# Kernel tuning notes

Hardware: AMD Instinct MI355X
Metric: run time of the kernel (lower is better)

## Reference

```python
import jax, jax.numpy as jnp
import numpy as np

B, S = 32, 4096
QRYDIM, CTXDIM, ENCDIM = 512, 512, 256


def setup_inputs() -> dict:
    key = jax.random.key(0)
    ks = jax.random.split(key, 8)
    qry = jax.random.normal(ks[0], (B, QRYDIM), dtype=jnp.float32)
    ctx = jax.random.normal(ks[1], (B, S, CTXDIM), dtype=jnp.float32)
    ctx_mask = jax.random.randint(ks[2], (B, S), 0, 2, dtype=jnp.int32)
    # first Linear(qrydim+ctxdim, encdim): split into ctx-part and qry-part
    # (equivalent to concat([ctx, qry]) @ W1^T since concat order is [ctx, qry])
    sc1 = 1.0 / np.sqrt(QRYDIM + CTXDIM)
    Wc = jax.random.uniform(ks[3], (CTXDIM, ENCDIM), jnp.float32, -sc1, sc1)
    Wq = jax.random.uniform(ks[4], (QRYDIM, ENCDIM), jnp.float32, -sc1, sc1)
    b1 = jax.random.uniform(ks[5], (ENCDIM,), jnp.float32, -sc1, sc1)
    sc2 = 1.0 / np.sqrt(ENCDIM)
    w2 = jax.random.uniform(ks[6], (ENCDIM,), jnp.float32, -sc2, sc2)
    b2 = jax.random.uniform(ks[7], (), jnp.float32, -sc2, sc2)
    return {"qry": qry, "ctx": ctx, "ctx_mask": ctx_mask,
            "Wc": Wc, "Wq": Wq, "b1": b1, "w2": w2, "b2": b2}


def reference(qry, ctx, ctx_mask, Wc, Wq, b1, w2, b2):
    # hidden = tanh(concat([ctx, qry_broadcast]) @ W1 + b1), computed without
    # materializing the (B, S, CTXDIM+QRYDIM) concat tensor
    h_ctx = jnp.einsum('bsc,ce->bse', ctx, Wc)          # (B, S, E)
    h_qry = jnp.einsum('bq,qe->be', qry, Wq)            # (B, E)
    h = jnp.tanh(h_ctx + h_qry[:, None, :] + b1)        # (B, S, E)
    scores = jnp.einsum('bse,e->bs', h, w2) + b2        # (B, S)
    # additive log-mask, then softmax over seqlen
    scores = scores + jnp.log(ctx_mask.astype(jnp.float32))
    alphas = jax.nn.softmax(scores, axis=-1)            # (B, S)
    # weighted sum over context (values default to ctx)
    summary = jnp.einsum('bs,bsd->bd', alphas, ctx)     # (B, CTXDIM)
    return alphas, summary, scores
```

## Files before the change

kernel.cpp:

```cpp
#include <hip/hip_runtime.h>
#include <math.h>

#define BB 32
#define SS 4096
#define CD 512
#define ED 256

#define ALPHAS_OFF 0
#define SUMMARY_OFF (BB * SS)
#define SCORES_OFF (BB * SS + BB * CD)

#define NEG_BIG (-1.0e30f)

typedef __attribute__((ext_vector_type(8))) short short8;
typedef __attribute__((ext_vector_type(8))) unsigned short us8;
typedef __attribute__((ext_vector_type(4))) float f32x4;

__device__ __forceinline__ unsigned short f2bf(float f) {
    unsigned u = __float_as_uint(f);
    u += 0x7FFFu + ((u >> 16) & 1u);
    return (unsigned short)(u >> 16);
}
__device__ __forceinline__ float bf2f(unsigned short h) {
    return __uint_as_float(((unsigned)h) << 16);
}
__device__ __forceinline__ float fast_tanh(float x) {
    const float ex = __expf(2.0f * x);
    return 1.0f - __fdividef(2.0f, ex + 1.0f);
}

#define WS_BH_OFF 32768
#define BPLANE 131072

__global__ void k_prep(const float* __restrict__ Wc, unsigned short* __restrict__ Bh,
                       unsigned short* __restrict__ Bl) {
    const int bid = blockIdx.x;
    const int l = threadIdx.x;
    const int e = (bid & 15) * 16 + (l & 15);
    const int kbase = (bid >> 4) * 32 + (l >> 4) * 8;
    const size_t off = ((size_t)bid * 64 + l) * 8;
#pragma unroll
    for (int j = 0; j < 8; ++j) {
        const float f = Wc[(size_t)(kbase + j) * ED + e];
        const unsigned short h = f2bf(f);
        Bh[off + j] = h;
        Bl[off + j] = f2bf(f - bf2f(h));
    }
}

__global__ void k_hq(const float* __restrict__ qry, const float* __restrict__ Wq,
                     const float* __restrict__ b1, float* __restrict__ hq) {
    const int b = blockIdx.x;
    const int e = threadIdx.x;
    __shared__ float qs[CD];
    qs[e] = qry[b * CD + e];
    qs[e + 256] = qry[b * CD + e + 256];
    __syncthreads();
    float acc = b1[e];
#pragma unroll 8
    for (int c = 0; c < CD; ++c) {
        acc = fmaf(qs[c], Wq[c * ED + e], acc);
    }
    hq[b * ED + e] = acc;
}

#define ST 64
__global__ __launch_bounds__(256, 3)
void k_scores(const float* __restrict__ ctx,
              const unsigned short* __restrict__ Bh, const unsigned short* __restrict__ Bl,
              const float* __restrict__ hq, const float* __restrict__ w2,
              const float* __restrict__ b2p, const int* __restrict__ mask,
              float* __restrict__ out) {
    const int b = blockIdx.y;
    const int s0 = blockIdx.x * ST;
    const int tid = threadIdx.x;
    const int w = tid >> 6;
    const int l = tid & 63;
    const int ehalf = w & 1;
    const int mhalf = w >> 1;

    __shared__ unsigned short AsH[2][4 * 64 * 8];
    __shared__ unsigned short AsL[2][4 * 64 * 8];
    __shared__ float red[2][ST];

    f32x4 acc[2][8];
#pragma unroll
    for (int mi = 0; mi < 2; ++mi)
#pragma unroll
        for (int t = 0; t < 8; ++t) acc[mi][t] = (f32x4)(0.0f);

    const float* ctx_b = ctx + (size_t)(b * SS + s0) * CD;

    const int amt = tid >> 6;
    const int alif = tid & 63;
    const int ar = amt * 16 + (alif & 15);
    const int akg = alif >> 4;
    const float* aptr = ctx_b + (size_t)ar * CD + akg * 8;

    const unsigned short* bhp = Bh + l * 8;
    const unsigned short* blp = Bl + l * 8;

    {
        const float4 v0 = *(const float4*)(aptr);
        const float4 v1 = *(const float4*)(aptr + 4);
        const float f[8] = {v0.x, v0.y, v0.z, v0.w, v1.x, v1.y, v1.z, v1.w};
        us8 H, L;
#pragma unroll
        for (int j = 0; j < 8; ++j) {
            const unsigned short h = f2bf(f[j]);
            H[j] = h;
            L[j] = f2bf(f[j] - bf2f(h));
        }
        *(us8*)(&AsH[0][tid * 8]) = H;
        *(us8*)(&AsL[0][tid * 8]) = L;
    }
    asm volatile("s_waitcnt lgkmcnt(0)" ::: "memory");
    __builtin_amdgcn_sched_barrier(0);
    __builtin_amdgcn_s_barrier();
    __builtin_amdgcn_sched_barrier(0);

    int cur = 0;
    for (int c = 0; c < 16; ++c) {
        float4 n0, n1;
        if (c < 15) {
            n0 = *(const float4*)(aptr + (c + 1) * 32);
            n1 = *(const float4*)(aptr + (c + 1) * 32 + 4);
        }

        short8 ah[2], alr[2];
#pragma unroll
        for (int mi = 0; mi < 2; ++mi) {
            const int aoff = ((mhalf * 2 + mi) * 64 + l) * 8;
            ah[mi] = *(const short8*)(&AsH[cur][aoff]);
            alr[mi] = *(const short8*)(&AsL[cur][aoff]);
        }

        __builtin_amdgcn_s_setprio(1);
#pragma unroll
        for (int et = 0; et < 8; ++et) {
            const int etile = ehalf * 8 + et;
            const size_t boff = (size_t)(c * 16 + etile) * 512;
            const short8 bh = *(const short8*)(bhp + boff);
            const short8 bl = *(const short8*)(blp + boff);
#pragma unroll
            for (int mi = 0; mi < 2; ++mi) {
                acc[mi][et] = __builtin_amdgcn_mfma_f32_16x16x32_bf16(ah[mi], bh, acc[mi][et], 0, 0, 0);
                acc[mi][et] = __builtin_amdgcn_mfma_f32_16x16x32_bf16(alr[mi], bh, acc[mi][et], 0, 0, 0);
                acc[mi][et] = __builtin_amdgcn_mfma_f32_16x16x32_bf16(ah[mi], bl, acc[mi][et], 0, 0, 0);
            }
        }
        __builtin_amdgcn_s_setprio(0);

        if (c < 15) {
            const float f[8] = {n0.x, n0.y, n0.z, n0.w, n1.x, n1.y, n1.z, n1.w};
            us8 H, L;
#pragma unroll
            for (int j = 0; j < 8; ++j) {
                const unsigned short h = f2bf(f[j]);
                H[j] = h;
                L[j] = f2bf(f[j] - bf2f(h));
            }
            *(us8*)(&AsH[cur ^ 1][tid * 8]) = H;
            *(us8*)(&AsL[cur ^ 1][tid * 8]) = L;
        }
        asm volatile("s_waitcnt lgkmcnt(0)" ::: "memory");
        __builtin_amdgcn_sched_barrier(0);
        __builtin_amdgcn_s_barrier();
        __builtin_amdgcn_sched_barrier(0);
        cur ^= 1;
    }

    float hqr[8], w2r[8];
#pragma unroll
    for (int t = 0; t < 8; ++t) {
        const int e = (ehalf * 8 + t) * 16 + (l & 15);
        hqr[t] = hq[b * ED + e];
        w2r[t] = w2[e];
    }

#pragma unroll
    for (int mi = 0; mi < 2; ++mi) {
#pragma unroll
        for (int reg = 0; reg < 4; ++reg) {
            float v = 0.0f;
#pragma unroll
            for (int t = 0; t < 8; ++t) {
                v += w2r[t] * fast_tanh(acc[mi][t][reg] + hqr[t]);
            }
            v += __shfl_xor(v, 1, 64);
            v += __shfl_xor(v, 2, 64);
            v += __shfl_xor(v, 4, 64);
            v += __shfl_xor(v, 8, 64);
            if ((l & 15) == 0) {
                const int row = (l >> 4) * 4 + reg;
                red[ehalf][(mhalf * 2 + mi) * 16 + row] = v;
            }
        }
    }
    __syncthreads();
    if (tid < ST) {
        const int s = s0 + tid;
        float sc = red[0][tid] + red[1][tid] + b2p[0];
        if (mask[b * SS + s] == 0) sc = NEG_BIG;
        out[SCORES_OFF + b * SS + s] = sc;
    }
}

__global__ void k_softmax(float* __restrict__ out) {
    const int b = blockIdx.x;
    const int tid = threadIdx.x;
    const float* sc = out + SCORES_OFF + b * SS;
    float* al = out + ALPHAS_OFF + b * SS;

    {
        float* sm = out + SUMMARY_OFF + b * CD;
        sm[tid] = 0.0f;
        sm[tid + 256] = 0.0f;
    }

    __shared__ float red[4];
    __shared__ float bcast;
    const int lane = tid & 63;
    const int wave = tid >> 6;

    float loc[16];
    float mx = -INFINITY;
#pragma unroll
    for (int i = 0; i < 16; ++i) {
        loc[i] = sc[i * 256 + tid];
        mx = fmaxf(mx, loc[i]);
    }
    for (int off = 32; off >= 1; off >>= 1) mx = fmaxf(mx, __shfl_down(mx, off, 64));
    if (lane == 0) red[wave] = mx;
    __syncthreads();
    if (tid == 0) bcast = fmaxf(fmaxf(red[0], red[1]), fmaxf(red[2], red[3]));
    __syncthreads();
    const float mxall = bcast;

    float sum = 0.0f;
#pragma unroll
    for (int i = 0; i < 16; ++i) {
        const float ev = __expf(loc[i] - mxall);
        loc[i] = ev;
        sum += ev;
    }
    for (int off = 32; off >= 1; off >>= 1) sum += __shfl_down(sum, off, 64);
    if (lane == 0) red[wave] = sum;
    __syncthreads();
    if (tid == 0) bcast = red[0] + red[1] + red[2] + red[3];
    __syncthreads();
    const float inv = 1.0f / bcast;

#pragma unroll
    for (int i = 0; i < 16; ++i) al[i * 256 + tid] = loc[i] * inv;
}

#define SROWS 128
__global__ void k_summary(const float* __restrict__ ctx, const float* __restrict__ out_alphas,
                          float* __restrict__ out) {
    const int b = blockIdx.y;
    const int s0 = blockIdx.x * SROWS;
    const int t = threadIdx.x;
    const int sg = t >> 7;
    const int d = (t & 127) * 4;

    __shared__ float al[SROWS];
    if (t < SROWS) al[t] = out_alphas[ALPHAS_OFF + b * SS + s0 + t];
    __syncthreads();

    const float* base = ctx + (size_t)(b * SS + s0 + sg * 64) * CD + d;
    const float* alp = &al[sg * 64];
    float4 a0 = make_float4(0.f, 0.f, 0.f, 0.f);
    float4 a1 = a0, a2 = a0, a3 = a0;
#pragma unroll 2
    for (int i = 0; i < 16; ++i) {
        const int s = i * 4;
        const float w0 = alp[s + 0], w1 = alp[s + 1], w2_ = alp[s + 2], w3 = alp[s + 3];
        if (w0 != 0.0f) {
            const float4 v0 = *(const float4*)(base + (size_t)(s + 0) * CD);
            a0.x = fmaf(w0, v0.x, a0.x); a0.y = fmaf(w0, v0.y, a0.y);
            a0.z = fmaf(w0, v0.z, a0.z); a0.w = fmaf(w0, v0.w, a0.w);
        }
        if (w1 != 0.0f) {
            const float4 v1 = *(const float4*)(base + (size_t)(s + 1) * CD);
            a1.x = fmaf(w1, v1.x, a1.x); a1.y = fmaf(w1, v1.y, a1.y);
            a1.z = fmaf(w1, v1.z, a1.z); a1.w = fmaf(w1, v1.w, a1.w);
        }
        if (w2_ != 0.0f) {
            const float4 v2 = *(const float4*)(base + (size_t)(s + 2) * CD);
            a2.x = fmaf(w2_, v2.x, a2.x); a2.y = fmaf(w2_, v2.y, a2.y);
            a2.z = fmaf(w2_, v2.z, a2.z); a2.w = fmaf(w2_, v2.w, a2.w);
        }
        if (w3 != 0.0f) {
            const float4 v3 = *(const float4*)(base + (size_t)(s + 3) * CD);
            a3.x = fmaf(w3, v3.x, a3.x); a3.y = fmaf(w3, v3.y, a3.y);
            a3.z = fmaf(w3, v3.z, a3.z); a3.w = fmaf(w3, v3.w, a3.w);
        }
    }
    const float rx = (a0.x + a1.x) + (a2.x + a3.x);
    const float ry = (a0.y + a1.y) + (a2.y + a3.y);
    const float rz = (a0.z + a1.z) + (a2.z + a3.z);
    const float rw = (a0.w + a1.w) + (a2.w + a3.w);
    float* dst = out + SUMMARY_OFF + b * CD + d;
    atomicAdd(dst + 0, rx);
    atomicAdd(dst + 1, ry);
    atomicAdd(dst + 2, rz);
    atomicAdd(dst + 3, rw);
}

extern "C" void kernel_launch(void* const* d_in, const int* in_sizes, int n_in,
                              void* d_out, int out_size, void* d_ws, size_t ws_size,
                              hipStream_t stream) {
    const float* qry  = (const float*)d_in[0];
    const float* ctx  = (const float*)d_in[1];
    const int*   msk  = (const int*)d_in[2];
    const float* Wc   = (const float*)d_in[3];
    const float* Wq   = (const float*)d_in[4];
    const float* b1   = (const float*)d_in[5];
    const float* w2   = (const float*)d_in[6];
    const float* b2   = (const float*)d_in[7];
    float* out = (float*)d_out;
    float* hq = (float*)d_ws;
    unsigned short* Bh = (unsigned short*)((char*)d_ws + WS_BH_OFF);
    unsigned short* Bl = Bh + BPLANE;

    k_prep<<<256, 64, 0, stream>>>(Wc, Bh, Bl);
    k_hq<<<BB, ED, 0, stream>>>(qry, Wq, b1, hq);
    k_scores<<<dim3(SS / ST, BB), 256, 0, stream>>>(ctx, Bh, Bl, hq, w2, b2, msk, out);
    k_softmax<<<BB, 256, 0, stream>>>(out);
    k_summary<<<dim3(SS / SROWS, BB), 256, 0, stream>>>(ctx, out, out);
}
```

Before: 522.9 us.

## Restructure score GEMM: register-resident A, LDS-staged weights via direct loads, split E across blocks

The scores kernel now keeps each wave's ctx rows in registers, converting them to bf16 hi/lo directly, and stages the Wc bf16 planes into LDS with global_load_lds async copies instead of reading them from global per wave. Each block covers 128 sequence rows and half the encoder dimension with 512 threads. The two E-halves combine their partial scores with atomicAdd into a scores buffer zeroed in k_hq, and bias and masking move into the softmax kernel. This trades the duplicated per-wave weight loads and the LDS round trip for ctx for atomics, and ctx is now read twice across the two E-half blocks.

```diff
diff --git a/kernel.cpp b/kernel.cpp
--- a/kernel.cpp
+++ b/kernel.cpp
@@ -28,6 +28,10 @@
     const float ex = __expf(2.0f * x);
     return 1.0f - __fdividef(2.0f, ex + 1.0f);
 }
+
+#define GLOAD_LDS16(g, l) __builtin_amdgcn_global_load_lds( \
+    (const __attribute__((address_space(1))) void*)(g),     \
+    (__attribute__((address_space(3))) void*)(l), 16, 0, 0)
 
 #define WS_BH_OFF 32768
 #define BPLANE 131072
@@ -49,9 +53,15 @@
 }
 
 __global__ void k_hq(const float* __restrict__ qry, const float* __restrict__ Wq,
-                     const float* __restrict__ b1, float* __restrict__ hq) {
+                     const float* __restrict__ b1, float* __restrict__ hq,
+                     float* __restrict__ out) {
     const int b = blockIdx.x;
     const int e = threadIdx.x;
+    {
+        float* scz = out + SCORES_OFF + b * SS;
+#pragma unroll
+        for (int i = 0; i < 16; ++i) scz[i * 256 + e] = 0.0f;
+    }
     __shared__ float qs[CD];
     qs[e] = qry[b * CD + e];
     qs[e + 256] = qry[b * CD + e + 256];
@@ -64,116 +74,122 @@
     hq[b * ED + e] = acc;
 }
 
-#define ST 64
-__global__ __launch_bounds__(256, 3)
+#define ST 128
+__global__ __launch_bounds__(512, 4)
 void k_scores(const float* __restrict__ ctx,
               const unsigned short* __restrict__ Bh, const unsigned short* __restrict__ Bl,
               const float* __restrict__ hq, const float* __restrict__ w2,
-              const float* __restrict__ b2p, const int* __restrict__ mask,
               float* __restrict__ out) {
     const int b = blockIdx.y;
-    const int s0 = blockIdx.x * ST;
+    const int stile = blockIdx.x >> 1;
+    const int ehalf = blockIdx.x & 1;
+    const int s0 = stile * ST;
     const int tid = threadIdx.x;
     const int w = tid >> 6;
     const int l = tid & 63;
-    const int ehalf = w & 1;
-    const int mhalf = w >> 1;
-
-    __shared__ unsigned short AsH[2][4 * 64 * 8];
-    __shared__ unsigned short AsL[2][4 * 64 * 8];
+    const int eq = w & 1;
+    const int mq = w >> 1;
+
+    __shared__ unsigned short BsH[2][8 * 64 * 8];
+    __shared__ unsigned short BsL[2][8 * 64 * 8];
     __shared__ float red[2][ST];
 
-    f32x4 acc[2][8];
+    f32x4 acc[2][4];
 #pragma unroll
     for (int mi = 0; mi < 2; ++mi)
 #pragma unroll
-        for (int t = 0; t < 8; ++t) acc[mi][t] = (f32x4)(0.0f);
+        for (int t = 0; t < 4; ++t) acc[mi][t] = (f32x4)(0.0f);
 
     const float* ctx_b = ctx + (size_t)(b * SS + s0) * CD;
 
-    const int amt = tid >> 6;
-    const int alif = tid & 63;
-    const int ar = amt * 16 + (alif & 15);
-    const int akg = alif >> 4;
-    const float* aptr = ctx_b + (size_t)ar * CD + akg * 8;
-
-    const unsigned short* bhp = Bh + l * 8;
-    const unsigned short* blp = Bl + l * 8;
-
+    const float* aptr0 = ctx_b + (size_t)(mq * 32 + (l & 15)) * CD + (l >> 4) * 8;
+    const float* aptr1 = aptr0 + 16 * CD;
+
+    const char* gBplane = (const char*)((w < 4) ? Bh : Bl);
+    char* lBbase = (char*)((w < 4) ? &BsH[0][0] : &BsL[0][0]);
+    const int wv = w & 3;
+    const int bq = wv * 2048 + l * 16;
+    const size_t gchunk0 = (size_t)(ehalf * 8) * 1024;
+
+    float4 ra0[2], ra1[2];
     {
-        const float4 v0 = *(const float4*)(aptr);
-        const float4 v1 = *(const float4*)(aptr + 4);
-        const float f[8] = {v0.x, v0.y, v0.z, v0.w, v1.x, v1.y, v1.z, v1.w};
-        us8 H, L;
-#pragma unroll
-        for (int j = 0; j < 8; ++j) {
-            const unsigned short h = f2bf(f[j]);
-            H[j] = h;
-            L[j] = f2bf(f[j] - bf2f(h));
-        }
-        *(us8*)(&AsH[0][tid * 8]) = H;
-        *(us8*)(&AsL[0][tid * 8]) = L;
-    }
-    asm volatile("s_waitcnt lgkmcnt(0)" ::: "memory");
+        const char* gsrc = gBplane + gchunk0 + bq;
+        GLOAD_LDS16(gsrc, lBbase + bq);
+        GLOAD_LDS16(gsrc + 1024, lBbase + bq + 1024);
+    }
+    __builtin_amdgcn_sched_barrier(0);
+    ra0[0] = *(const float4*)(aptr0);
+    ra1[0] = *(const float4*)(aptr0 + 4);
+    ra0[1] = *(const float4*)(aptr1);
+    ra1[1] = *(const float4*)(aptr1 + 4);
+    __builtin_amdgcn_sched_barrier(0);
+    asm volatile("s_waitcnt vmcnt(4)" ::: "memory");
     __builtin_amdgcn_sched_barrier(0);
     __builtin_amdgcn_s_barrier();
     __builtin_amdgcn_sched_barrier(0);
 
     int cur = 0;
     for (int c = 0; c < 16; ++c) {
-        float4 n0, n1;
-        if (c < 15) {
-            n0 = *(const float4*)(aptr + (c + 1) * 32);
-            n1 = *(const float4*)(aptr + (c + 1) * 32 + 4);
-        }
-
-        short8 ah[2], alr[2];
+        short8 ah[2], alo[2];
 #pragma unroll
         for (int mi = 0; mi < 2; ++mi) {
-            const int aoff = ((mhalf * 2 + mi) * 64 + l) * 8;
-            ah[mi] = *(const short8*)(&AsH[cur][aoff]);
-            alr[mi] = *(const short8*)(&AsL[cur][aoff]);
-        }
-
-        __builtin_amdgcn_s_setprio(1);
-#pragma unroll
-        for (int et = 0; et < 8; ++et) {
-            const int etile = ehalf * 8 + et;
-            const size_t boff = (size_t)(c * 16 + etile) * 512;
-            const short8 bh = *(const short8*)(bhp + boff);
-            const short8 bl = *(const short8*)(blp + boff);
-#pragma unroll
-            for (int mi = 0; mi < 2; ++mi) {
-                acc[mi][et] = __builtin_amdgcn_mfma_f32_16x16x32_bf16(ah[mi], bh, acc[mi][et], 0, 0, 0);
-                acc[mi][et] = __builtin_amdgcn_mfma_f32_16x16x32_bf16(alr[mi], bh, acc[mi][et], 0, 0, 0);
-                acc[mi][et] = __builtin_amdgcn_mfma_f32_16x16x32_bf16(ah[mi], bl, acc[mi][et], 0, 0, 0);
-            }
-        }
-        __builtin_amdgcn_s_setprio(0);
-
-        if (c < 15) {
-            const float f[8] = {n0.x, n0.y, n0.z, n0.w, n1.x, n1.y, n1.z, n1.w};
-            us8 H, L;
+            const float f[8] = {ra0[mi].x, ra0[mi].y, ra0[mi].z, ra0[mi].w,
+                                ra1[mi].x, ra1[mi].y, ra1[mi].z, ra1[mi].w};
+            short8 H, L;
 #pragma unroll
             for (int j = 0; j < 8; ++j) {
                 const unsigned short h = f2bf(f[j]);
-                H[j] = h;
-                L[j] = f2bf(f[j] - bf2f(h));
+                H[j] = (short)h;
+                L[j] = (short)f2bf(f[j] - bf2f(h));
             }
-            *(us8*)(&AsH[cur ^ 1][tid * 8]) = H;
-            *(us8*)(&AsL[cur ^ 1][tid * 8]) = L;
-        }
-        asm volatile("s_waitcnt lgkmcnt(0)" ::: "memory");
+            ah[mi] = H;
+            alo[mi] = L;
+        }
+        __builtin_amdgcn_sched_barrier(0);
+
+        if (c < 15) {
+            const char* gsrc = gBplane + (size_t)(c + 1) * 16384 + gchunk0 + bq;
+            char* ldst = lBbase + (cur ^ 1) * 8192 + bq;
+            GLOAD_LDS16(gsrc, ldst);
+            GLOAD_LDS16(gsrc + 1024, ldst + 1024);
+        }
+        __builtin_amdgcn_sched_barrier(0);
+        if (c < 15) {
+            ra0[0] = *(const float4*)(aptr0 + (c + 1) * 32);
+            ra1[0] = *(const float4*)(aptr0 + (c + 1) * 32 + 4);
+            ra0[1] = *(const float4*)(aptr1 + (c + 1) * 32);
+            ra1[1] = *(const float4*)(aptr1 + (c + 1) * 32 + 4);
+        }
+        __builtin_amdgcn_sched_barrier(0);
+
+        __builtin_amdgcn_s_setprio(1);
+#pragma unroll
+        for (int t = 0; t < 4; ++t) {
+            const int le = eq * 4 + t;
+            const int boff = (le * 64 + l) * 8;
+            const short8 bh = *(const short8*)(&BsH[cur][boff]);
+            const short8 bl = *(const short8*)(&BsL[cur][boff]);
+#pragma unroll
+            for (int mi = 0; mi < 2; ++mi) {
+                acc[mi][t] = __builtin_amdgcn_mfma_f32_16x16x32_bf16(ah[mi], bh, acc[mi][t], 0, 0, 0);
+                acc[mi][t] = __builtin_amdgcn_mfma_f32_16x16x32_bf16(alo[mi], bh, acc[mi][t], 0, 0, 0);
+                acc[mi][t] = __builtin_amdgcn_mfma_f32_16x16x32_bf16(ah[mi], bl, acc[mi][t], 0, 0, 0);
+            }
+        }
+        __builtin_amdgcn_s_setprio(0);
+
+        __builtin_amdgcn_sched_barrier(0);
+        asm volatile("s_waitcnt vmcnt(4)" ::: "memory");
         __builtin_amdgcn_sched_barrier(0);
         __builtin_amdgcn_s_barrier();
         __builtin_amdgcn_sched_barrier(0);
         cur ^= 1;
     }
 
-    float hqr[8], w2r[8];
-#pragma unroll
-    for (int t = 0; t < 8; ++t) {
-        const int e = (ehalf * 8 + t) * 16 + (l & 15);
+    float hqr[4], w2r[4];
+#pragma unroll
+    for (int t = 0; t < 4; ++t) {
+        const int e = (ehalf * 8 + eq * 4 + t) * 16 + (l & 15);
         hqr[t] = hq[b * ED + e];
         w2r[t] = w2[e];
     }
@@ -184,7 +200,7 @@
         for (int reg = 0; reg < 4; ++reg) {
             float v = 0.0f;
 #pragma unroll
-            for (int t = 0; t < 8; ++t) {
+            for (int t = 0; t < 4; ++t) {
                 v += w2r[t] * fast_tanh(acc[mi][t][reg] + hqr[t]);
             }
             v += __shfl_xor(v, 1, 64);
@@ -193,23 +209,21 @@
             v += __shfl_xor(v, 8, 64);
             if ((l & 15) == 0) {
                 const int row = (l >> 4) * 4 + reg;
-                red[ehalf][(mhalf * 2 + mi) * 16 + row] = v;
+                red[eq][(mq * 2 + mi) * 16 + row] = v;
             }
         }
     }
     __syncthreads();
     if (tid < ST) {
-        const int s = s0 + tid;
-        float sc = red[0][tid] + red[1][tid] + b2p[0];
-        if (mask[b * SS + s] == 0) sc = NEG_BIG;
-        out[SCORES_OFF + b * SS + s] = sc;
-    }
-}
-
-__global__ void k_softmax(float* __restrict__ out) {
+        atomicAdd(out + SCORES_OFF + b * SS + s0 + tid, red[0][tid] + red[1][tid]);
+    }
+}
+
+__global__ void k_softmax(float* __restrict__ out, const int* __restrict__ mask,
+                          const float* __restrict__ b2p) {
     const int b = blockIdx.x;
     const int tid = threadIdx.x;
-    const float* sc = out + SCORES_OFF + b * SS;
+    float* sc = out + SCORES_OFF + b * SS;
     float* al = out + ALPHAS_OFF + b * SS;
 
     {
@@ -218,6 +232,8 @@
         sm[tid + 256] = 0.0f;
     }
 
+    const float b2v = b2p[0];
+
     __shared__ float red[4];
     __shared__ float bcast;
     const int lane = tid & 63;
@@ -227,8 +243,12 @@
     float mx = -INFINITY;
 #pragma unroll
     for (int i = 0; i < 16; ++i) {
-        loc[i] = sc[i * 256 + tid];
-        mx = fmaxf(mx, loc[i]);
+        const int s = i * 256 + tid;
+        float v = sc[s] + b2v;
+        if (mask[b * SS + s] == 0) v = NEG_BIG;
+        sc[s] = v;
+        loc[i] = v;
+        mx = fmaxf(mx, v);
     }
     for (int off = 32; off >= 1; off >>= 1) mx = fmaxf(mx, __shfl_down(mx, off, 64));
     if (lane == 0) red[wave] = mx;
@@ -325,8 +345,8 @@
     unsigned short* Bl = Bh + BPLANE;
 
     k_prep<<<256, 64, 0, stream>>>(Wc, Bh, Bl);
-    k_hq<<<BB, ED, 0, stream>>>(qry, Wq, b1, hq);
-    k_scores<<<dim3(SS / ST, BB), 256, 0, stream>>>(ctx, Bh, Bl, hq, w2, b2, msk, out);
-    k_softmax<<<BB, 256, 0, stream>>>(out);
+    k_hq<<<BB, ED, 0, stream>>>(qry, Wq, b1, hq, out);
+    k_scores<<<dim3(64, BB), 512, 0, stream>>>(ctx, Bh, Bl, hq, w2, out);
+    k_softmax<<<BB, 256, 0, stream>>>(out, msk, b2);
     k_summary<<<dim3(SS / SROWS, BB), 256, 0, stream>>>(ctx, out, out);
 }
```

Result: faster. 510.2 us (-2.4%).
